# Optimization experiments

Hardware: AMD Instinct MI355X
Metric: run time of the kernel (lower is better)

The kernel has to match this reference:

```python
import jax, jax.numpy as jnp
import numpy as np

B, T, C, E = 8, 2048, 2048, 16
DE = C // E          # per-expert width = 128
H = 4 * DE           # expert hidden = 512


def setup_inputs() -> dict:
    key = jax.random.key(0)
    ks = jax.random.split(key, 7)
    s = 0.02
    return {
        "x": jax.random.normal(ks[0], (B, T, C), dtype=jnp.float32),
        "gate_w": jax.random.normal(ks[1], (E, C), dtype=jnp.float32) * s,
        "gate_b": jnp.zeros((E,), dtype=jnp.float32),
        "fc_w": jax.random.normal(ks[2], (E, H, DE), dtype=jnp.float32) * s,
        "fc_b": jnp.zeros((E, H), dtype=jnp.float32),
        "proj_w": jax.random.normal(ks[3], (E, DE, H), dtype=jnp.float32) * s,
        "proj_b": jnp.zeros((E, DE), dtype=jnp.float32),
    }


def _thres_hot(logits):
    # ThresHot: hard threshold at 0 with straight-through gradient.
    hard = (logits > 0).astype(logits.dtype)
    return logits + jax.lax.stop_gradient(hard - logits)


def reference(x, gate_w, gate_b, fc_w, fc_b, proj_w, proj_b):
    b, t, c = x.shape
    e = gate_b.shape[0]
    de = c // e
    # gate: [b,t,E]
    logits = jnp.einsum("btc,ec->bte", x, gate_w) + gate_b
    gw = _thres_hot(logits)
    # chunk channels: expert index is the FASTEST-varying dim (torch view(b,t,de,E))
    xc = x.reshape(b, t, de, e)  # [b,t,de,E]
    # per-expert MLP: fc -> gelu(exact) -> proj  (dropout=0)
    h = jnp.einsum("btde,ehd->bteh", xc, fc_w) + fc_b          # [b,t,E,H]
    h = jax.nn.gelu(h, approximate=False)
    out = jnp.einsum("bteh,edh->bted", h, proj_w) + proj_b      # [b,t,E,de]
    # weighted combine; torch stacks experts at dim=2 then flattens (de fastest)
    return (gw[..., None] * out).reshape(b, t, c)
```

## Files before the change

### kernel.cpp

```cpp
#include <hip/hip_runtime.h>

#define N_TOK 16384
#define C_DIM 2048
#define E_NUM 16
#define DE_DIM 128
#define H_DIM 512

typedef __attribute__((ext_vector_type(8))) short bf16x8;
typedef __attribute__((ext_vector_type(4))) float f32x4;

__device__ __forceinline__ unsigned short f2bf(float f) {
    unsigned int u = __float_as_uint(f);
    unsigned int r = u + 0x7fffu + ((u >> 16) & 1u);
    return (unsigned short)(r >> 16);
}

__device__ __forceinline__ uint4 pack8(float4 a, float4 b) {
    return make_uint4(
        (unsigned int)f2bf(a.x) | ((unsigned int)f2bf(a.y) << 16),
        (unsigned int)f2bf(a.z) | ((unsigned int)f2bf(a.w) << 16),
        (unsigned int)f2bf(b.x) | ((unsigned int)f2bf(b.y) << 16),
        (unsigned int)f2bf(b.z) | ((unsigned int)f2bf(b.w) << 16));
}

__device__ __forceinline__ float gelu_erf(float v) {
    float z  = v * 0.70710678118654752f;
    float az = fabsf(z);
    float t  = __builtin_amdgcn_rcpf(1.0f + 0.3275911f * az);
    float poly = t * (0.254829592f + t * (-0.284496736f + t * (1.421413741f +
                 t * (-1.453152027f + t * 1.061405429f))));
    float ex = __expf(-z * z);
    float er = copysignf(1.0f - poly * ex, z);
    return 0.5f * v * (1.0f + er);
}

__global__ __launch_bounds__(256) void moe_conv_w(
    const float* __restrict__ fcw, const float* __restrict__ pjw,
    unsigned short* __restrict__ fcwb, unsigned short* __restrict__ pjwb)
{
    const int id = blockIdx.x * 256 + threadIdx.x;
    {
        const int base = id * 8;
        const int d0 = base & 127;
        const int h  = (base >> 7) & 511;
        const int dd = d0 ^ ((h & 7) << 3);
        float4 a = *reinterpret_cast<const float4*>(fcw + base);
        float4 b = *reinterpret_cast<const float4*>(fcw + base + 4);
        *reinterpret_cast<uint4*>(fcwb + (base & ~127) + dd) = pack8(a, b);
    }
    {
        const int base = id * 8;
        const int h0 = base & 511;
        const int d  = (base >> 9) & 127;
        const int hh = h0 ^ ((d & 7) << 3);
        float4 a = *reinterpret_cast<const float4*>(pjw + base);
        float4 b = *reinterpret_cast<const float4*>(pjw + base + 4);
        *reinterpret_cast<uint4*>(pjwb + (base & ~511) + hh) = pack8(a, b);
    }
}

__global__ __launch_bounds__(256) void moe_gate(
    const float* __restrict__ xg,
    const float* __restrict__ gw,
    const float* __restrict__ gb,
    float* __restrict__ gwf)
{
    __shared__ float gws[16 * 256];

    const int t  = threadIdx.x;
    const int n0 = blockIdx.x * 16;
    const int nl = t >> 4;
    const int p  = t & 15;

    double dacc[16];
#pragma unroll
    for (int e = 0; e < 16; ++e) dacc[e] = 0.0;

    for (int cc = 0; cc < 8; ++cc) {
        __syncthreads();
#pragma unroll
        for (int ii = 0; ii < 4; ++ii) {
            int fi = ii * 1024 + t * 4;
            int e = fi >> 8, cl = fi & 255;
            *reinterpret_cast<float4*>(&gws[e * 256 + cl]) =
                *reinterpret_cast<const float4*>(gw + (size_t)e * 2048 + cc * 256 + cl);
        }
        __syncthreads();
#pragma unroll
        for (int g = 0; g < 4; ++g) {
            const int cl = g * 64 + p * 4;
            float4 xa = *reinterpret_cast<const float4*>(
                xg + (size_t)(n0 + nl) * 2048 + cc * 256 + cl);
            double xd0 = xa.x, xd1 = xa.y, xd2 = xa.z, xd3 = xa.w;
#pragma unroll
            for (int e = 0; e < 16; ++e) {
                float4 ga = *reinterpret_cast<const float4*>(&gws[e * 256 + cl]);
                double s = dacc[e];
                s = fma(xd0, (double)ga.x, s);
                s = fma(xd1, (double)ga.y, s);
                s = fma(xd2, (double)ga.z, s);
                s = fma(xd3, (double)ga.w, s);
                dacc[e] = s;
            }
        }
    }
#pragma unroll
    for (int e = 0; e < 16; ++e) {
        double v = dacc[e];
        v += __shfl_xor(v, 1);
        v += __shfl_xor(v, 2);
        v += __shfl_xor(v, 4);
        v += __shfl_xor(v, 8);
        dacc[e] = v;
    }
    if (p == 0) {
        float g[16];
#pragma unroll
        for (int e = 0; e < 16; ++e)
            g[e] = (dacc[e] + (double)gb[e] > 0.0) ? 1.0f : 0.0f;
        float4* o = reinterpret_cast<float4*>(gwf + (size_t)(n0 + nl) * 16);
        o[0] = make_float4(g[0],  g[1],  g[2],  g[3]);
        o[1] = make_float4(g[4],  g[5],  g[6],  g[7]);
        o[2] = make_float4(g[8],  g[9],  g[10], g[11]);
        o[3] = make_float4(g[12], g[13], g[14], g[15]);
    }
}

template<int PRE>
__global__ __launch_bounds__(256, 2) void moe_expert_mlp(
    const float* __restrict__ xg,
    const float* __restrict__ fcw,
    const float* __restrict__ fcb,
    const float* __restrict__ pjw,
    const float* __restrict__ pjb,
    const unsigned short* __restrict__ fcwb,
    const unsigned short* __restrict__ pjwb,
    const float* __restrict__ gwf,
    float* __restrict__ y)
{
    constexpr int W1S = PRE ? 128 : 136;
    constexpr int W2S = PRE ? 64  : 72;
    __shared__ unsigned short W1s[64 * W1S];
    __shared__ unsigned short W2s[128 * W2S];
    __shared__ unsigned short Hs[4 * 32 * 72];

    const int t    = threadIdx.x;
    const int wid  = t >> 6;
    const int lane = t & 63;
    const int q    = lane >> 4;
    const int m    = lane & 15;
    const int raw = blockIdx.x;
    const int e   = (raw >> 3) & 15;
    const int tb  = (raw & 7) | ((raw >> 7) << 3);
    const int n0  = tb * 128 + wid * 32;

    bf16x8 a1[2][4];
#pragma unroll
    for (int tm = 0; tm < 2; ++tm)
#pragma unroll
        for (int kk = 0; kk < 4; ++kk) {
            const float* base = xg + (size_t)(n0 + tm * 16 + m) * 2048
                              + (kk * 32 + q * 8) * 16 + e;
            union { unsigned short u[8]; bf16x8 v; } pk;
#pragma unroll
            for (int j = 0; j < 8; ++j) pk.u[j] = f2bf(base[j * 16]);
            a1[tm][kk] = pk.v;
        }

    f32x4 oacc[2][8];
#pragma unroll
    for (int tm = 0; tm < 2; ++tm)
#pragma unroll
        for (int tn = 0; tn < 8; ++tn) oacc[tm][tn] = (f32x4){0.f, 0.f, 0.f, 0.f};

    unsigned short* HsW = &Hs[wid * 32 * 72];
    const char* W1b = reinterpret_cast<const char*>(W1s);
    const char* W2b = reinterpret_cast<const char*>(W2s);

    for (int hc = 0; hc < 8; ++hc) {
        __syncthreads();
        if constexpr (PRE) {
            const unsigned short* g1 = fcwb + ((size_t)e * 512 + hc * 64) * 128;
            const unsigned short* g2 = pjwb + (size_t)e * 128 * 512 + hc * 64;
#pragma unroll
            for (int it = 0; it < 4; ++it) {
                const int s = it * 2048 + t * 8;
                __builtin_amdgcn_global_load_lds(
                    (const __attribute__((address_space(1))) unsigned int*)(g1 + s),
                    (__attribute__((address_space(3))) unsigned int*)(&W1s[s]), 16, 0, 0);
            }
#pragma unroll
            for (int it = 0; it < 4; ++it) {
                const int s = it * 2048 + t * 8;
                __builtin_amdgcn_global_load_lds(
                    (const __attribute__((address_space(1))) unsigned int*)
                        (g2 + (size_t)(s >> 6) * 512 + (s & 63)),
                    (__attribute__((address_space(3))) unsigned int*)(&W2s[s]), 16, 0, 0);
            }
        } else {
#pragma unroll
            for (int it = 0; it < 4; ++it) {
                int idx = it * 256 + t;
                int hh = idx >> 4, ds = (idx & 15) * 8;
                const float* src = fcw + ((size_t)e * 512 + hc * 64 + hh) * 128 + ds;
                float4 va = *reinterpret_cast<const float4*>(src);
                float4 vb = *reinterpret_cast<const float4*>(src + 4);
                *reinterpret_cast<uint4*>(&W1s[hh * W1S + ds]) = pack8(va, vb);
            }
#pragma unroll
            for (int it = 0; it < 4; ++it) {
                int idx = it * 256 + t;
                int d = idx >> 3, cs = (idx & 7) * 8;
                const float* src = pjw + ((size_t)e * 128 + d) * 512 + hc * 64 + cs;
                float4 va = *reinterpret_cast<const float4*>(src);
                float4 vb = *reinterpret_cast<const float4*>(src + 4);
                *reinterpret_cast<uint4*>(&W2s[d * W2S + cs]) = pack8(va, vb);
            }
        }
        __syncthreads();

        f32x4 h1[2][4];
#pragma unroll
        for (int tm = 0; tm < 2; ++tm)
#pragma unroll
            for (int tn = 0; tn < 4; ++tn) h1[tm][tn] = (f32x4){0.f, 0.f, 0.f, 0.f};
#pragma unroll
        for (int kk = 0; kk < 4; ++kk) {
#pragma unroll
            for (int tn = 0; tn < 4; ++tn) {
                bf16x8 b;
                if constexpr (PRE) {
                    const int r = tn * 16 + m;
                    b = *reinterpret_cast<const bf16x8*>(
                        W1b + r * 256 + (((kk * 32 + q * 8) * 2) ^ ((r & 7) << 4)));
                } else {
                    b = *reinterpret_cast<const bf16x8*>(
                        &W1s[(tn * 16 + m) * W1S + kk * 32 + q * 8]);
                }
                h1[0][tn] = __builtin_amdgcn_mfma_f32_16x16x32_bf16(a1[0][kk], b, h1[0][tn], 0, 0, 0);
                h1[1][tn] = __builtin_amdgcn_mfma_f32_16x16x32_bf16(a1[1][kk], b, h1[1][tn], 0, 0, 0);
            }
        }
#pragma unroll
        for (int tn = 0; tn < 4; ++tn) {
            float bias = fcb[e * 512 + hc * 64 + tn * 16 + m];
#pragma unroll
            for (int tm = 0; tm < 2; ++tm)
#pragma unroll
                for (int r = 0; r < 4; ++r) {
                    float g = gelu_erf(h1[tm][tn][r] + bias);
                    HsW[(tm * 16 + q * 4 + r) * 72 + tn * 16 + m] = f2bf(g);
                }
        }
        __asm__ volatile("" ::: "memory");

#pragma unroll
        for (int kk2 = 0; kk2 < 2; ++kk2) {
            bf16x8 a2_0 = *reinterpret_cast<const bf16x8*>(&HsW[(m) * 72 + kk2 * 32 + q * 8]);
            bf16x8 a2_1 = *reinterpret_cast<const bf16x8*>(&HsW[(16 + m) * 72 + kk2 * 32 + q * 8]);
#pragma unroll
            for (int tn2 = 0; tn2 < 8; ++tn2) {
                bf16x8 b2;
                if constexpr (PRE) {
                    const int r2 = tn2 * 16 + m;
                    b2 = *reinterpret_cast<const bf16x8*>(
                        W2b + r2 * 128 + (((kk2 * 32 + q * 8) * 2) ^ ((r2 & 7) << 4)));
                } else {
                    b2 = *reinterpret_cast<const bf16x8*>(
                        &W2s[(tn2 * 16 + m) * W2S + kk2 * 32 + q * 8]);
                }
                oacc[0][tn2] = __builtin_amdgcn_mfma_f32_16x16x32_bf16(a2_0, b2, oacc[0][tn2], 0, 0, 0);
                oacc[1][tn2] = __builtin_amdgcn_mfma_f32_16x16x32_bf16(a2_1, b2, oacc[1][tn2], 0, 0, 0);
            }
        }
    }

    float gwv[2][4];
#pragma unroll
    for (int tm = 0; tm < 2; ++tm)
#pragma unroll
        for (int r = 0; r < 4; ++r)
            gwv[tm][r] = gwf[(size_t)(n0 + tm * 16 + q * 4 + r) * 16 + e];
#pragma unroll
    for (int tn2 = 0; tn2 < 8; ++tn2) {
        float pb = pjb[e * 128 + tn2 * 16 + m];
#pragma unroll
        for (int tm = 0; tm < 2; ++tm)
#pragma unroll
            for (int r = 0; r < 4; ++r) {
                float v = (oacc[tm][tn2][r] + pb) * gwv[tm][r];
                y[(size_t)(n0 + tm * 16 + q * 4 + r) * 2048 + e * 128 + tn2 * 16 + m] = v;
            }
    }
}

extern "C" void kernel_launch(void* const* d_in, const int* in_sizes, int n_in,
                              void* d_out, int out_size, void* d_ws, size_t ws_size,
                              hipStream_t stream) {
    const float* x      = (const float*)d_in[0];
    const float* gate_w = (const float*)d_in[1];
    const float* gate_b = (const float*)d_in[2];
    const float* fc_w   = (const float*)d_in[3];
    const float* fc_b   = (const float*)d_in[4];
    const float* proj_w = (const float*)d_in[5];
    const float* proj_b = (const float*)d_in[6];
    float* y            = (float*)d_out;

    const size_t gwf_bytes = (size_t)N_TOK * E_NUM * 4;
    const size_t wb_bytes  = (size_t)E_NUM * H_DIM * DE_DIM * 2;
    float* gwf = (float*)d_ws;
    unsigned short* fcwb = (unsigned short*)((char*)d_ws + gwf_bytes);
    unsigned short* pjwb = (unsigned short*)((char*)d_ws + gwf_bytes + wb_bytes);
    const int use_pre = (ws_size >= gwf_bytes + 2 * wb_bytes) ? 1 : 0;

    if (use_pre)
        moe_conv_w<<<dim3(512), dim3(256), 0, stream>>>(fc_w, proj_w, fcwb, pjwb);
    moe_gate<<<dim3(N_TOK / 16), dim3(256), 0, stream>>>(x, gate_w, gate_b, gwf);
    if (use_pre)
        moe_expert_mlp<1><<<dim3(E_NUM * (N_TOK / 128)), dim3(256), 0, stream>>>(
            x, fc_w, fc_b, proj_w, proj_b, fcwb, pjwb, gwf, y);
    else
        moe_expert_mlp<0><<<dim3(E_NUM * (N_TOK / 128)), dim3(256), 0, stream>>>(
            x, fc_w, fc_b, proj_w, proj_b, fcwb, pjwb, gwf, y);
}
```

Measured before the change: 452.0 us.

## Use fp32 gate accumulation with fp64 fallback and register-prefetch expert weights

After: 568.7 us. 1.26x slower.

```diff
diff --git a/kernel.cpp b/kernel.cpp
--- a/kernel.cpp
+++ b/kernel.cpp
@@ -72,9 +72,9 @@
     const int nl = t >> 4;
     const int p  = t & 15;
 
-    double dacc[16];
-#pragma unroll
-    for (int e = 0; e < 16; ++e) dacc[e] = 0.0;
+    float facc[16];
+#pragma unroll
+    for (int e = 0; e < 16; ++e) facc[e] = 0.0f;
 
     for (int cc = 0; cc < 8; ++cc) {
         __syncthreads();
@@ -91,39 +91,47 @@
             const int cl = g * 64 + p * 4;
             float4 xa = *reinterpret_cast<const float4*>(
                 xg + (size_t)(n0 + nl) * 2048 + cc * 256 + cl);
-            double xd0 = xa.x, xd1 = xa.y, xd2 = xa.z, xd3 = xa.w;
 #pragma unroll
             for (int e = 0; e < 16; ++e) {
                 float4 ga = *reinterpret_cast<const float4*>(&gws[e * 256 + cl]);
-                double s = dacc[e];
-                s = fma(xd0, (double)ga.x, s);
-                s = fma(xd1, (double)ga.y, s);
-                s = fma(xd2, (double)ga.z, s);
-                s = fma(xd3, (double)ga.w, s);
-                dacc[e] = s;
+                float s = facc[e];
+                s = fmaf(xa.x, ga.x, s);
+                s = fmaf(xa.y, ga.y, s);
+                s = fmaf(xa.z, ga.z, s);
+                s = fmaf(xa.w, ga.w, s);
+                facc[e] = s;
             }
         }
     }
 #pragma unroll
     for (int e = 0; e < 16; ++e) {
-        double v = dacc[e];
+        float v = facc[e];
         v += __shfl_xor(v, 1);
         v += __shfl_xor(v, 2);
         v += __shfl_xor(v, 4);
         v += __shfl_xor(v, 8);
-        dacc[e] = v;
-    }
-    if (p == 0) {
-        float g[16];
-#pragma unroll
-        for (int e = 0; e < 16; ++e)
-            g[e] = (dacc[e] + (double)gb[e] > 0.0) ? 1.0f : 0.0f;
-        float4* o = reinterpret_cast<float4*>(gwf + (size_t)(n0 + nl) * 16);
-        o[0] = make_float4(g[0],  g[1],  g[2],  g[3]);
-        o[1] = make_float4(g[4],  g[5],  g[6],  g[7]);
-        o[2] = make_float4(g[8],  g[9],  g[10], g[11]);
-        o[3] = make_float4(g[12], g[13], g[14], g[15]);
-    }
+        facc[e] = v;
+    }
+    const float l = facc[p] + gb[p];
+    float dec;
+    if (fabsf(l) >= 1e-3f) {
+        dec = (l > 0.0f) ? 1.0f : 0.0f;
+    } else {
+        const float* xr = xg + (size_t)(n0 + nl) * 2048;
+        const float* gr = gw + (size_t)p * 2048;
+        double s0 = 0.0, s1 = 0.0, s2 = 0.0, s3 = 0.0;
+        for (int c = 0; c < 2048; c += 4) {
+            float4 xv = *reinterpret_cast<const float4*>(xr + c);
+            float4 gv = *reinterpret_cast<const float4*>(gr + c);
+            s0 = fma((double)xv.x, (double)gv.x, s0);
+            s1 = fma((double)xv.y, (double)gv.y, s1);
+            s2 = fma((double)xv.z, (double)gv.z, s2);
+            s3 = fma((double)xv.w, (double)gv.w, s3);
+        }
+        double sd = ((s0 + s1) + (s2 + s3)) + (double)gb[p];
+        dec = (sd > 0.0) ? 1.0f : 0.0f;
+    }
+    gwf[(size_t)(n0 + nl) * 16 + p] = dec;
 }
 
 template<int PRE>
@@ -177,25 +185,38 @@
     const char* W1b = reinterpret_cast<const char*>(W1s);
     const char* W2b = reinterpret_cast<const char*>(W2s);
 
+    uint4 w1r[4], w2r[4];
+    if constexpr (PRE) {
+#pragma unroll
+        for (int it = 0; it < 4; ++it) {
+            const int s = it * 2048 + t * 8;
+            w1r[it] = *reinterpret_cast<const uint4*>(
+                fcwb + ((size_t)e * 512 + 0 * 64) * 128 + s);
+            w2r[it] = *reinterpret_cast<const uint4*>(
+                pjwb + (size_t)e * 128 * 512 + 0 * 64
+                     + (size_t)(s >> 6) * 512 + (s & 63));
+        }
+    }
+
     for (int hc = 0; hc < 8; ++hc) {
         __syncthreads();
         if constexpr (PRE) {
-            const unsigned short* g1 = fcwb + ((size_t)e * 512 + hc * 64) * 128;
-            const unsigned short* g2 = pjwb + (size_t)e * 128 * 512 + hc * 64;
 #pragma unroll
             for (int it = 0; it < 4; ++it) {
                 const int s = it * 2048 + t * 8;
-                __builtin_amdgcn_global_load_lds(
-                    (const __attribute__((address_space(1))) unsigned int*)(g1 + s),
-                    (__attribute__((address_space(3))) unsigned int*)(&W1s[s]), 16, 0, 0);
-            }
-#pragma unroll
-            for (int it = 0; it < 4; ++it) {
-                const int s = it * 2048 + t * 8;
-                __builtin_amdgcn_global_load_lds(
-                    (const __attribute__((address_space(1))) unsigned int*)
-                        (g2 + (size_t)(s >> 6) * 512 + (s & 63)),
-                    (__attribute__((address_space(3))) unsigned int*)(&W2s[s]), 16, 0, 0);
+                *reinterpret_cast<uint4*>(&W1s[s]) = w1r[it];
+                *reinterpret_cast<uint4*>(&W2s[s]) = w2r[it];
+            }
+            if (hc < 7) {
+                const unsigned short* g1 = fcwb + ((size_t)e * 512 + (hc + 1) * 64) * 128;
+                const unsigned short* g2 = pjwb + (size_t)e * 128 * 512 + (hc + 1) * 64;
+#pragma unroll
+                for (int it = 0; it < 4; ++it) {
+                    const int s = it * 2048 + t * 8;
+                    w1r[it] = *reinterpret_cast<const uint4*>(g1 + s);
+                    w2r[it] = *reinterpret_cast<const uint4*>(
+                        g2 + (size_t)(s >> 6) * 512 + (s & 63));
+                }
             }
         } else {
 #pragma unroll
```

## Fuse gate computation into expert MLP kernel with fp32 and fp64 fallback

Applied to the files above, without the earlier changes.

Result: slower. 516.7 us (+14.3%).

```diff
diff --git a/kernel.cpp b/kernel.cpp
--- a/kernel.cpp
+++ b/kernel.cpp
@@ -59,83 +59,17 @@
     }
 }
 
-__global__ __launch_bounds__(256) void moe_gate(
+template<int PRE>
+__global__ __launch_bounds__(256, 3) void moe_expert_mlp(
     const float* __restrict__ xg,
     const float* __restrict__ gw,
     const float* __restrict__ gb,
-    float* __restrict__ gwf)
-{
-    __shared__ float gws[16 * 256];
-
-    const int t  = threadIdx.x;
-    const int n0 = blockIdx.x * 16;
-    const int nl = t >> 4;
-    const int p  = t & 15;
-
-    double dacc[16];
-#pragma unroll
-    for (int e = 0; e < 16; ++e) dacc[e] = 0.0;
-
-    for (int cc = 0; cc < 8; ++cc) {
-        __syncthreads();
-#pragma unroll
-        for (int ii = 0; ii < 4; ++ii) {
-            int fi = ii * 1024 + t * 4;
-            int e = fi >> 8, cl = fi & 255;
-            *reinterpret_cast<float4*>(&gws[e * 256 + cl]) =
-                *reinterpret_cast<const float4*>(gw + (size_t)e * 2048 + cc * 256 + cl);
-        }
-        __syncthreads();
-#pragma unroll
-        for (int g = 0; g < 4; ++g) {
-            const int cl = g * 64 + p * 4;
-            float4 xa = *reinterpret_cast<const float4*>(
-                xg + (size_t)(n0 + nl) * 2048 + cc * 256 + cl);
-            double xd0 = xa.x, xd1 = xa.y, xd2 = xa.z, xd3 = xa.w;
-#pragma unroll
-            for (int e = 0; e < 16; ++e) {
-                float4 ga = *reinterpret_cast<const float4*>(&gws[e * 256 + cl]);
-                double s = dacc[e];
-                s = fma(xd0, (double)ga.x, s);
-                s = fma(xd1, (double)ga.y, s);
-                s = fma(xd2, (double)ga.z, s);
-                s = fma(xd3, (double)ga.w, s);
-                dacc[e] = s;
-            }
-        }
-    }
-#pragma unroll
-    for (int e = 0; e < 16; ++e) {
-        double v = dacc[e];
-        v += __shfl_xor(v, 1);
-        v += __shfl_xor(v, 2);
-        v += __shfl_xor(v, 4);
-        v += __shfl_xor(v, 8);
-        dacc[e] = v;
-    }
-    if (p == 0) {
-        float g[16];
-#pragma unroll
-        for (int e = 0; e < 16; ++e)
-            g[e] = (dacc[e] + (double)gb[e] > 0.0) ? 1.0f : 0.0f;
-        float4* o = reinterpret_cast<float4*>(gwf + (size_t)(n0 + nl) * 16);
-        o[0] = make_float4(g[0],  g[1],  g[2],  g[3]);
-        o[1] = make_float4(g[4],  g[5],  g[6],  g[7]);
-        o[2] = make_float4(g[8],  g[9],  g[10], g[11]);
-        o[3] = make_float4(g[12], g[13], g[14], g[15]);
-    }
-}
-
-template<int PRE>
-__global__ __launch_bounds__(256, 2) void moe_expert_mlp(
-    const float* __restrict__ xg,
     const float* __restrict__ fcw,
     const float* __restrict__ fcb,
     const float* __restrict__ pjw,
     const float* __restrict__ pjb,
     const unsigned short* __restrict__ fcwb,
     const unsigned short* __restrict__ pjwb,
-    const float* __restrict__ gwf,
     float* __restrict__ y)
 {
     constexpr int W1S = PRE ? 128 : 136;
@@ -153,6 +87,47 @@
     const int e   = (raw >> 3) & 15;
     const int tb  = (raw & 7) | ((raw >> 7) << 3);
     const int n0  = tb * 128 + wid * 32;
+
+    float4 gwr[8];
+#pragma unroll
+    for (int c = 0; c < 8; ++c)
+        gwr[c] = *reinterpret_cast<const float4*>(
+            gw + (size_t)e * 2048 + c * 256 + lane * 4);
+    const float gbe = gb[e];
+    unsigned int gmask = 0;
+#pragma unroll 2
+    for (int tk = 0; tk < 32; ++tk) {
+        const float* xr = xg + (size_t)(n0 + tk) * 2048 + lane * 4;
+        float4 xv[8];
+#pragma unroll
+        for (int c = 0; c < 8; ++c)
+            xv[c] = *reinterpret_cast<const float4*>(xr + c * 256);
+        float s = 0.f;
+#pragma unroll
+        for (int c = 0; c < 8; ++c) {
+            s = fmaf(xv[c].x, gwr[c].x, s);
+            s = fmaf(xv[c].y, gwr[c].y, s);
+            s = fmaf(xv[c].z, gwr[c].z, s);
+            s = fmaf(xv[c].w, gwr[c].w, s);
+        }
+        s += __shfl_xor(s, 1);  s += __shfl_xor(s, 2);  s += __shfl_xor(s, 4);
+        s += __shfl_xor(s, 8);  s += __shfl_xor(s, 16); s += __shfl_xor(s, 32);
+        float l = s + gbe;
+        if (__builtin_expect(fabsf(l) < 1e-3f, 0)) {
+            double d = 0.0;
+#pragma unroll
+            for (int c = 0; c < 8; ++c) {
+                d = fma((double)xv[c].x, (double)gwr[c].x, d);
+                d = fma((double)xv[c].y, (double)gwr[c].y, d);
+                d = fma((double)xv[c].z, (double)gwr[c].z, d);
+                d = fma((double)xv[c].w, (double)gwr[c].w, d);
+            }
+            d += __shfl_xor(d, 1);  d += __shfl_xor(d, 2);  d += __shfl_xor(d, 4);
+            d += __shfl_xor(d, 8);  d += __shfl_xor(d, 16); d += __shfl_xor(d, 32);
+            l = (d + (double)gbe > 0.0) ? 1.f : -1.f;
+        }
+        gmask |= (l > 0.f ? 1u : 0u) << tk;
+    }
 
     bf16x8 a1[2][4];
 #pragma unroll
@@ -275,12 +250,6 @@
         }
     }
 
-    float gwv[2][4];
-#pragma unroll
-    for (int tm = 0; tm < 2; ++tm)
-#pragma unroll
-        for (int r = 0; r < 4; ++r)
-            gwv[tm][r] = gwf[(size_t)(n0 + tm * 16 + q * 4 + r) * 16 + e];
 #pragma unroll
     for (int tn2 = 0; tn2 < 8; ++tn2) {
         float pb = pjb[e * 128 + tn2 * 16 + m];
@@ -288,8 +257,10 @@
         for (int tm = 0; tm < 2; ++tm)
 #pragma unroll
             for (int r = 0; r < 4; ++r) {
-                float v = (oacc[tm][tn2][r] + pb) * gwv[tm][r];
-                y[(size_t)(n0 + tm * 16 + q * 4 + r) * 2048 + e * 128 + tn2 * 16 + m] = v;
+                const int tok = tm * 16 + q * 4 + r;
+                float gv = ((gmask >> tok) & 1u) ? 1.0f : 0.0f;
+                float v = (oacc[tm][tn2][r] + pb) * gv;
+                y[(size_t)(n0 + tok) * 2048 + e * 128 + tn2 * 16 + m] = v;
             }
     }
 }
@@ -306,20 +277,17 @@
     const float* proj_b = (const float*)d_in[6];
     float* y            = (float*)d_out;
 
-    const size_t gwf_bytes = (size_t)N_TOK * E_NUM * 4;
     const size_t wb_bytes  = (size_t)E_NUM * H_DIM * DE_DIM * 2;
-    float* gwf = (float*)d_ws;
-    unsigned short* fcwb = (unsigned short*)((char*)d_ws + gwf_bytes);
-    unsigned short* pjwb = (unsigned short*)((char*)d_ws + gwf_bytes + wb_bytes);
-    const int use_pre = (ws_size >= gwf_bytes + 2 * wb_bytes) ? 1 : 0;
-
-    if (use_pre)
+    unsigned short* fcwb = (unsigned short*)d_ws;
+    unsigned short* pjwb = (unsigned short*)((char*)d_ws + wb_bytes);
+    const int use_pre = (ws_size >= 2 * wb_bytes) ? 1 : 0;
+
+    if (use_pre) {
         moe_conv_w<<<dim3(512), dim3(256), 0, stream>>>(fc_w, proj_w, fcwb, pjwb);
-    moe_gate<<<dim3(N_TOK / 16), dim3(256), 0, stream>>>(x, gate_w, gate_b, gwf);
-    if (use_pre)
         moe_expert_mlp<1><<<dim3(E_NUM * (N_TOK / 128)), dim3(256), 0, stream>>>(
-            x, fc_w, fc_b, proj_w, proj_b, fcwb, pjwb, gwf, y);
-    else
+            x, gate_w, gate_b, fc_w, fc_b, proj_w, proj_b, fcwb, pjwb, y);
+    } else {
         moe_expert_mlp<0><<<dim3(E_NUM * (N_TOK / 128)), dim3(256), 0, stream>>>(
-            x, fc_w, fc_b, proj_w, proj_b, fcwb, pjwb, gwf, y);
-}
+            x, gate_w, gate_b, fc_w, fc_b, proj_w, proj_b, fcwb, pjwb, y);
+    }
+}
```
